# Kernel optimization log

Hardware: AMD Instinct MI355X
Metric: run time of the kernel (lower is better)

The kernel has to match this reference:

```python
import jax, jax.numpy as jnp
import numpy as np

B, D, T, BINS = 8, 768, 16384, 1024

def setup_inputs() -> dict:
    key = jax.random.key(0)
    k1, k2, k3, k4 = jax.random.split(key, 4)
    ssl_content = jax.random.normal(k1, (B, D, T), dtype=jnp.float32)
    conv_w = jax.random.normal(k2, (D, D, 2), dtype=jnp.float32) * 0.02  # Conv1d(768,768,k=2,s=2) weight [out,in,k]
    conv_b = jax.random.normal(k3, (D,), dtype=jnp.float32) * 0.02
    codebook = jax.random.normal(k4, (BINS, D), dtype=jnp.float32)
    return {"ssl_content": ssl_content, "conv_w": conv_w, "conv_b": conv_b, "codebook": codebook}

def reference(ssl_content, conv_w, conv_b, codebook):
    # ssl_proj: Conv1d(D, D, kernel_size=2, stride=2), no padding
    ssl = jax.lax.conv_general_dilated(
        ssl_content, conv_w, window_strides=(2,), padding='VALID',
        dimension_numbers=('NCH', 'OIH', 'NCH')) + conv_b[None, :, None]  # [B, D, T//2]
    x = jnp.transpose(ssl, (0, 2, 1))            # b d n -> b n d : [B, T', D]
    b, tq, d = x.shape
    flat = x.reshape(-1, d)                      # [B*T', D]
    # Euclidean codebook search: argmin_k ||flat - codebook[k]||^2
    d2 = (jnp.sum(flat * flat, axis=-1, keepdims=True)
          - 2.0 * (flat @ codebook.T)
          + jnp.sum(codebook * codebook, axis=-1))  # [B*T', BINS]
    codes = jnp.argmin(d2, axis=-1).reshape(b, tq)  # n_q=1 -> indices for quantizer 0: [B, T']
    prompt = codes[0][None, :]                   # codes[0,0].unsqueeze(0) -> [1, T']
    return prompt
```

## Files before the change

kernel.cpp:

```cpp
#include <hip/hip_runtime.h>

#define D    768
#define T    16384
#define TQ   8192
#define BINS 1024
#define K1   1536
#define NKA  (K1 / 32)
#define NKS  (D / 32)
#define FRAG 1024

typedef _Float16 f16;
typedef _Float16 h8 __attribute__((ext_vector_type(8)));
typedef float    f32x4 __attribute__((ext_vector_type(4)));


__device__ __forceinline__ void gl_lds16(const void* g, void* l) {
    __builtin_amdgcn_global_load_lds(
        (const __attribute__((address_space(1))) void*)g,
        (__attribute__((address_space(3))) void*)l, 16, 0, 0);
}

__global__ __launch_bounds__(64) void cnorm_kernel(const float* __restrict__ cb,
                                                   float* __restrict__ cnorm) {
    int bin  = blockIdx.x;
    int lane = threadIdx.x;
    const float* row = cb + bin * D;
    float s = 0.f;
    for (int k = lane; k < D; k += 64) { float v = row[k]; s += v * v; }
    #pragma unroll
    for (int off = 32; off > 0; off >>= 1) s += __shfl_down(s, off);
    if (lane == 0) cnorm[bin] = s;
}

__global__ __launch_bounds__(256) void pack_b_kernel(
    const float* __restrict__ src, f16* __restrict__ hi, f16* __restrict__ lo,
    int K, int nfrag) {
    int wid = threadIdx.x >> 6, lane = threadIdx.x & 63;
    int fid = blockIdx.x * 4 + wid;
    if (fid >= nfrag) return;
    int nk = K >> 5;
    int r16 = fid / nk, kblk = fid - r16 * nk;
    int row = r16 * 16 + (lane & 15);
    int k0  = kblk * 32 + 8 * (lane >> 4);
    const float* s = src + (size_t)row * K + k0;
    float4 v0 = *(const float4*)s;
    float4 v1 = *(const float4*)(s + 4);
    float vv[8] = {v0.x, v0.y, v0.z, v0.w, v1.x, v1.y, v1.z, v1.w};
    h8 vh, vl;
    #pragma unroll
    for (int j = 0; j < 8; ++j) {
        f16 h = (f16)vv[j];
        vh[j] = h;
        vl[j] = (f16)((vv[j] - (float)h) * 2048.f);
    }
    size_t off = ((size_t)fid * 64 + lane) * 8;
    *(h8*)&hi[off] = vh;
    *(h8*)&lo[off] = vl;
}

__global__ __launch_bounds__(256) void pack_a_kernel(const float* __restrict__ ssl,
                                                     f16* __restrict__ hi,
                                                     f16* __restrict__ lo) {
    int wid = threadIdx.x >> 6, lane = threadIdx.x & 63;
    int kblk = blockIdx.x;
    int l15 = lane & 15, lk = lane >> 4;
    #pragma unroll
    for (int q = 0; q < 2; ++q) {
        int tblk = blockIdx.y * 8 + wid * 2 + q;
        int tp = tblk * 16 + l15;
        int i0 = kblk * 16 + 4 * lk;
        float vv[8];
        #pragma unroll
        for (int ii = 0; ii < 4; ++ii) {
            float2 v = *(const float2*)&ssl[(size_t)(i0 + ii) * T + 2 * tp];
            vv[2 * ii]     = v.x;
            vv[2 * ii + 1] = v.y;
        }
        h8 vh, vl;
        #pragma unroll
        for (int j = 0; j < 8; ++j) {
            f16 h = (f16)vv[j];
            vh[j] = h;
            vl[j] = (f16)((vv[j] - (float)h) * 2048.f);
        }
        size_t off = ((size_t)(tblk * NKA + kblk) * 64 + lane) * 8;
        *(h8*)&hi[off] = vh;
        *(h8*)&lo[off] = vl;
    }
}

__global__ __launch_bounds__(256, 2) void conv_mfma_kernel(
    const f16* __restrict__ Ah, const f16* __restrict__ Al,
    const f16* __restrict__ Bh, const f16* __restrict__ Bl,
    const float* __restrict__ bias,
    f16* __restrict__ Xhi, f16* __restrict__ Xlo)
{
    __shared__ __align__(16) char smem[65536];
    int tid = threadIdx.x, lane = tid & 63, wid = tid >> 6;
    int wm = wid >> 1, wn = wid & 1;
    int l15 = lane & 15, lk = lane >> 4;
    int mb = blockIdx.y * 128, nb = blockIdx.x * 128;
    int mb16 = mb >> 4, nb16 = nb >> 4;

    const f16* gsrc; int blk16;
    if      (wid == 0) { gsrc = Ah; blk16 = mb16; }
    else if (wid == 1) { gsrc = Al; blk16 = mb16; }
    else if (wid == 2) { gsrc = Bh; blk16 = nb16; }
    else               { gsrc = Bl; blk16 = nb16; }
    const char* gw = (const char*)gsrc + (size_t)blk16 * NKA * FRAG + lane * 16;
    char* lw0 = smem + wid * 8192;
    char* lw1 = smem + 32768 + wid * 8192;

    const f32x4 zero4 = {0.f, 0.f, 0.f, 0.f};
    f32x4 acc[4][4], acc2[4][4];
    #pragma unroll
    for (int i = 0; i < 4; ++i)
        #pragma unroll
        for (int j = 0; j < 4; ++j) { acc[i][j] = zero4; acc2[i][j] = zero4; }

    #pragma unroll
    for (int f = 0; f < 8; ++f)
        gl_lds16(gw + (size_t)(f * NKA) * FRAG, lw0 + f * FRAG);
    __syncthreads();

    int cur = 0;
    for (int kblk = 0; kblk < NKA; ++kblk) {
        if (kblk + 1 < NKA) {
            char* lwn = cur ? lw0 : lw1;
            #pragma unroll
            for (int f = 0; f < 8; ++f)
                gl_lds16(gw + (size_t)(f * NKA + kblk + 1) * FRAG, lwn + f * FRAG);
        }
        const char* base = smem + cur * 32768;
        h8 ah[4], al[4];
        #pragma unroll
        for (int mf = 0; mf < 4; ++mf) {
            int fo = (wm * 4 + mf) * FRAG + lane * 16;
            ah[mf] = *(const h8*)(base + fo);
            al[mf] = *(const h8*)(base + 8192 + fo);
        }
        #pragma unroll
        for (int nf = 0; nf < 4; ++nf) {
            int fo = (wn * 4 + nf) * FRAG + lane * 16;
            h8 bh = *(const h8*)(base + 16384 + fo);
            h8 bl = *(const h8*)(base + 24576 + fo);
            #pragma unroll
            for (int mf = 0; mf < 4; ++mf) {
                acc [mf][nf] = __builtin_amdgcn_mfma_f32_16x16x32_f16(ah[mf], bh, acc [mf][nf], 0, 0, 0);
                acc2[mf][nf] = __builtin_amdgcn_mfma_f32_16x16x32_f16(ah[mf], bl, acc2[mf][nf], 0, 0, 0);
                acc2[mf][nf] = __builtin_amdgcn_mfma_f32_16x16x32_f16(al[mf], bh, acc2[mf][nf], 0, 0, 0);
            }
        }
        __syncthreads();
        cur ^= 1;
    }

    float* sb = (float*)smem;
    float bv[4];
    #pragma unroll
    for (int nf = 0; nf < 4; ++nf) bv[nf] = bias[nb + wn * 64 + nf * 16 + l15];
    #pragma unroll
    for (int s = 0; s < 4; ++s) {
        __syncthreads();
        if (wm == (s >> 1)) {
            #pragma unroll
            for (int mh = 0; mh < 2; ++mh) {
                int mf = (s & 1) * 2 + mh;
                int srow = mh * 16 + lk * 4;
                #pragma unroll
                for (int nf = 0; nf < 4; ++nf) {
                    int scol = wn * 64 + nf * 16 + l15;
                    #pragma unroll
                    for (int r = 0; r < 4; ++r)
                        sb[(srow + r) * 132 + scol] =
                            acc[mf][nf][r] + acc2[mf][nf][r] * 4.8828125e-4f + bv[nf];
                }
            }
        }
        __syncthreads();
        #pragma unroll
        for (int h = 0; h < 2; ++h) {
            int f = wid * 2 + h;
            int tl = f & 1, dbl = f >> 1;
            int srow = tl * 16 + l15;
            int sd   = dbl * 32 + 8 * lk;
            float vv[8];
            #pragma unroll
            for (int j = 0; j < 8; ++j) vv[j] = sb[srow * 132 + sd + j];
            h8 vh, vl;
            #pragma unroll
            for (int j = 0; j < 8; ++j) {
                f16 hh = (f16)vv[j];
                vh[j] = hh;
                vl[j] = (f16)((vv[j] - (float)hh) * 2048.f);
            }
            int tblk_g = mb16 + s * 2 + tl;
            int dblk_g = (nb >> 5) + dbl;
            size_t off = ((size_t)(tblk_g * NKS + dblk_g) * 64 + lane) * 8;
            *(h8*)&Xhi[off] = vh;
            *(h8*)&Xlo[off] = vl;
        }
    }
}

__global__ __launch_bounds__(256, 2) void score_mfma_kernel(
    const f16* __restrict__ Ah, const f16* __restrict__ Al,
    const f16* __restrict__ Bh, const f16* __restrict__ Bl,
    const float* __restrict__ cnorm,
    float* __restrict__ pval, int* __restrict__ pidx)
{
    __shared__ __align__(16) char smem[65536];
    int tid = threadIdx.x, lane = tid & 63, wid = tid >> 6;
    int wm = wid >> 1, wn = wid & 1;
    int l15 = lane & 15, lk = lane >> 4;
    int mb = blockIdx.y * 128, nb = blockIdx.x * 128;
    int mb16 = mb >> 4, nb16 = nb >> 4;

    const f16* gsrc; int blk16;
    if      (wid == 0) { gsrc = Ah; blk16 = mb16; }
    else if (wid == 1) { gsrc = Al; blk16 = mb16; }
    else if (wid == 2) { gsrc = Bh; blk16 = nb16; }
    else               { gsrc = Bl; blk16 = nb16; }
    const char* gw = (const char*)gsrc + (size_t)blk16 * NKS * FRAG + lane * 16;
    char* lw0 = smem + wid * 8192;
    char* lw1 = smem + 32768 + wid * 8192;

    const f32x4 zero4 = {0.f, 0.f, 0.f, 0.f};
    f32x4 acc[4][4], acc2[4][4];
    #pragma unroll
    for (int i = 0; i < 4; ++i)
        #pragma unroll
        for (int j = 0; j < 4; ++j) { acc[i][j] = zero4; acc2[i][j] = zero4; }

    #pragma unroll
    for (int f = 0; f < 8; ++f)
        gl_lds16(gw + (size_t)(f * NKS) * FRAG, lw0 + f * FRAG);
    __syncthreads();

    int cur = 0;
    for (int kblk = 0; kblk < NKS; ++kblk) {
        if (kblk + 1 < NKS) {
            char* lwn = cur ? lw0 : lw1;
            #pragma unroll
            for (int f = 0; f < 8; ++f)
                gl_lds16(gw + (size_t)(f * NKS + kblk + 1) * FRAG, lwn + f * FRAG);
        }
        const char* base = smem + cur * 32768;
        h8 ah[4], al[4];
        #pragma unroll
        for (int mf = 0; mf < 4; ++mf) {
            int fo = (wm * 4 + mf) * FRAG + lane * 16;
            ah[mf] = *(const h8*)(base + fo);
            al[mf] = *(const h8*)(base + 8192 + fo);
        }
        #pragma unroll
        for (int nf = 0; nf < 4; ++nf) {
            int fo = (wn * 4 + nf) * FRAG + lane * 16;
            h8 bh = *(const h8*)(base + 16384 + fo);
            h8 bl = *(const h8*)(base + 24576 + fo);
            #pragma unroll
            for (int mf = 0; mf < 4; ++mf) {
                acc [mf][nf] = __builtin_amdgcn_mfma_f32_16x16x32_f16(ah[mf], bh, acc [mf][nf], 0, 0, 0);
                acc2[mf][nf] = __builtin_amdgcn_mfma_f32_16x16x32_f16(ah[mf], bl, acc2[mf][nf], 0, 0, 0);
                acc2[mf][nf] = __builtin_amdgcn_mfma_f32_16x16x32_f16(al[mf], bh, acc2[mf][nf], 0, 0, 0);
            }
        }
        __syncthreads();
        cur ^= 1;
    }
    float cn[4];
    #pragma unroll
    for (int nf = 0; nf < 4; ++nf) cn[nf] = cnorm[nb + wn * 64 + nf * 16 + l15];
    int slice = blockIdx.x * 2 + wn;
    #pragma unroll
    for (int mf = 0; mf < 4; ++mf) {
        #pragma unroll
        for (int r = 0; r < 4; ++r) {
            float v = 3.4e38f; int ix = 0;
            #pragma unroll
            for (int nf = 0; nf < 4; ++nf) {
                float dot = acc[mf][nf][r] + acc2[mf][nf][r] * 4.8828125e-4f;
                float sc = cn[nf] - 2.f * dot;
                int col = nb + wn * 64 + nf * 16 + l15;
                if (sc < v) { v = sc; ix = col; }
            }
            #pragma unroll
            for (int off = 8; off > 0; off >>= 1) {
                float ov = __shfl_xor(v, off);
                int   oi = __shfl_xor(ix, off);
                if (ov < v || (ov == v && oi < ix)) { v = ov; ix = oi; }
            }
            if (l15 == 0) {
                int row = mb + wm * 64 + mf * 16 + lk * 4 + r;
                pval[row * 16 + slice] = v;
                pidx[row * 16 + slice] = ix;
            }
        }
    }
}

__global__ __launch_bounds__(256) void argmin_final_kernel(
    const float* __restrict__ pval, const int* __restrict__ pidx,
    int* __restrict__ out)
{
    int r = blockIdx.x * 256 + threadIdx.x;
    float best = 3.4e38f; int bi = 0;
    #pragma unroll
    for (int s = 0; s < 16; ++s) {
        float v = pval[r * 16 + s];
        if (v < best) { best = v; bi = pidx[r * 16 + s]; }
    }
    out[r] = bi;
}

extern "C" void kernel_launch(void* const* d_in, const int* in_sizes, int n_in,
                              void* d_out, int out_size, void* d_ws, size_t ws_size,
                              hipStream_t stream) {
    const float* ssl = (const float*)d_in[0];
    const float* W   = (const float*)d_in[1];
    const float* bia = (const float*)d_in[2];
    const float* cb  = (const float*)d_in[3];
    int* out = (int*)d_out;

    char* p = (char*)d_ws;
    float* cnorm = (float*)p;  p += 4096;
    f16* Whi  = (f16*)p;  p += (size_t)D * K1 * 2;
    f16* Wlo  = (f16*)p;  p += (size_t)D * K1 * 2;
    f16* CBhi = (f16*)p;  p += (size_t)BINS * D * 2;
    f16* CBlo = (f16*)p;  p += (size_t)BINS * D * 2;
    f16* Ahi  = (f16*)p;  p += (size_t)TQ * K1 * 2;
    f16* Alo  = (f16*)p;  p += (size_t)TQ * K1 * 2;
    f16* Xhi  = (f16*)p;  p += (size_t)TQ * D * 2;
    f16* Xlo  = (f16*)p;  p += (size_t)TQ * D * 2;
    float* pval = (float*)p;  p += (size_t)TQ * 16 * 4;
    int*   pidx = (int*)p;    p += (size_t)TQ * 16 * 4;

    cnorm_kernel<<<BINS, 64, 0, stream>>>(cb, cnorm);
    pack_b_kernel<<<(48 * 48) / 4, 256, 0, stream>>>(W, Whi, Wlo, K1, 48 * 48);
    pack_b_kernel<<<(64 * 24) / 4, 256, 0, stream>>>(cb, CBhi, CBlo, D, 64 * 24);
    pack_a_kernel<<<dim3(NKA, TQ / 128), 256, 0, stream>>>(ssl, Ahi, Alo);
    conv_mfma_kernel<<<dim3(D / 128, TQ / 128), 256, 0, stream>>>(
        Ahi, Alo, Whi, Wlo, bia, Xhi, Xlo);
    score_mfma_kernel<<<dim3(BINS / 128, TQ / 128), 256, 0, stream>>>(
        Xhi, Xlo, CBhi, CBlo, cnorm, pval, pidx);
    argmin_final_kernel<<<TQ / 256, 256, 0, stream>>>(pval, pidx, out);
}
```

Before: 562.0 us.

## Merge prep kernels into one launch and swizzle GEMM block order

Combines the codebook-norm kernel, both B-packing kernels and the A-packing kernel into a single prep kernel that branches on block index, replacing four launches with one. It also remaps the block indices of the conv and score GEMM kernels so that consecutive workgroups are spread across the grid, likely to change L2/MALL locality and how work lands on XCDs. The cost is extra branching in the prep kernel and a different locality pattern that may help or hurt cache reuse.

```diff
diff --git a/kernel.cpp b/kernel.cpp
--- a/kernel.cpp
+++ b/kernel.cpp
@@ -9,6 +9,12 @@
 #define NKS  (D / 32)
 #define FRAG 1024
 
+#define NFRAG_W  ((D / 16) * NKA)
+#define NFRAG_CB ((BINS / 16) * NKS)
+#define NB_PACKB ((NFRAG_W + NFRAG_CB) / 4)
+#define NB_PACKA (NKA * (TQ / 128))
+#define NB_CNORM (BINS / 4)
+
 typedef _Float16 f16;
 typedef _Float16 h8 __attribute__((ext_vector_type(8)));
 typedef float    f32x4 __attribute__((ext_vector_type(4)));
@@ -20,62 +26,29 @@
         (__attribute__((address_space(3))) void*)l, 16, 0, 0);
 }
 
-__global__ __launch_bounds__(64) void cnorm_kernel(const float* __restrict__ cb,
-                                                   float* __restrict__ cnorm) {
-    int bin  = blockIdx.x;
-    int lane = threadIdx.x;
-    const float* row = cb + bin * D;
-    float s = 0.f;
-    for (int k = lane; k < D; k += 64) { float v = row[k]; s += v * v; }
-    #pragma unroll
-    for (int off = 32; off > 0; off >>= 1) s += __shfl_down(s, off);
-    if (lane == 0) cnorm[bin] = s;
-}
-
-__global__ __launch_bounds__(256) void pack_b_kernel(
-    const float* __restrict__ src, f16* __restrict__ hi, f16* __restrict__ lo,
-    int K, int nfrag) {
+__global__ __launch_bounds__(256) void prep_kernel(
+    const float* __restrict__ ssl, const float* __restrict__ W,
+    const float* __restrict__ cb,
+    f16* __restrict__ Whi, f16* __restrict__ Wlo,
+    f16* __restrict__ CBhi, f16* __restrict__ CBlo,
+    f16* __restrict__ Ahi, f16* __restrict__ Alo,
+    float* __restrict__ cnorm)
+{
+    int b = blockIdx.x;
     int wid = threadIdx.x >> 6, lane = threadIdx.x & 63;
-    int fid = blockIdx.x * 4 + wid;
-    if (fid >= nfrag) return;
-    int nk = K >> 5;
-    int r16 = fid / nk, kblk = fid - r16 * nk;
-    int row = r16 * 16 + (lane & 15);
-    int k0  = kblk * 32 + 8 * (lane >> 4);
-    const float* s = src + (size_t)row * K + k0;
-    float4 v0 = *(const float4*)s;
-    float4 v1 = *(const float4*)(s + 4);
-    float vv[8] = {v0.x, v0.y, v0.z, v0.w, v1.x, v1.y, v1.z, v1.w};
-    h8 vh, vl;
-    #pragma unroll
-    for (int j = 0; j < 8; ++j) {
-        f16 h = (f16)vv[j];
-        vh[j] = h;
-        vl[j] = (f16)((vv[j] - (float)h) * 2048.f);
-    }
-    size_t off = ((size_t)fid * 64 + lane) * 8;
-    *(h8*)&hi[off] = vh;
-    *(h8*)&lo[off] = vl;
-}
-
-__global__ __launch_bounds__(256) void pack_a_kernel(const float* __restrict__ ssl,
-                                                     f16* __restrict__ hi,
-                                                     f16* __restrict__ lo) {
-    int wid = threadIdx.x >> 6, lane = threadIdx.x & 63;
-    int kblk = blockIdx.x;
-    int l15 = lane & 15, lk = lane >> 4;
-    #pragma unroll
-    for (int q = 0; q < 2; ++q) {
-        int tblk = blockIdx.y * 8 + wid * 2 + q;
-        int tp = tblk * 16 + l15;
-        int i0 = kblk * 16 + 4 * lk;
-        float vv[8];
-        #pragma unroll
-        for (int ii = 0; ii < 4; ++ii) {
-            float2 v = *(const float2*)&ssl[(size_t)(i0 + ii) * T + 2 * tp];
-            vv[2 * ii]     = v.x;
-            vv[2 * ii + 1] = v.y;
-        }
+
+    if (b < NB_PACKB) {
+        int fid = b * 4 + wid;
+        const float* src; f16* hi; f16* lo; int K, nk, fidl;
+        if (fid < NFRAG_W) { src = W;  hi = Whi;  lo = Wlo;  K = K1; nk = NKA; fidl = fid; }
+        else               { src = cb; hi = CBhi; lo = CBlo; K = D;  nk = NKS; fidl = fid - NFRAG_W; }
+        int r16 = fidl / nk, kblk = fidl - r16 * nk;
+        int row = r16 * 16 + (lane & 15);
+        int k0  = kblk * 32 + 8 * (lane >> 4);
+        const float* s = src + (size_t)row * K + k0;
+        float4 v0 = *(const float4*)s;
+        float4 v1 = *(const float4*)(s + 4);
+        float vv[8] = {v0.x, v0.y, v0.z, v0.w, v1.x, v1.y, v1.z, v1.w};
         h8 vh, vl;
         #pragma unroll
         for (int j = 0; j < 8; ++j) {
@@ -83,9 +56,44 @@
             vh[j] = h;
             vl[j] = (f16)((vv[j] - (float)h) * 2048.f);
         }
-        size_t off = ((size_t)(tblk * NKA + kblk) * 64 + lane) * 8;
+        size_t off = ((size_t)fidl * 64 + lane) * 8;
         *(h8*)&hi[off] = vh;
         *(h8*)&lo[off] = vl;
+    } else if (b < NB_PACKB + NB_PACKA) {
+        int idx = b - NB_PACKB;
+        int kblk = idx % NKA, yb = idx / NKA;
+        int l15 = lane & 15, lk = lane >> 4;
+        #pragma unroll
+        for (int q = 0; q < 2; ++q) {
+            int tblk = yb * 8 + wid * 2 + q;
+            int tp = tblk * 16 + l15;
+            int i0 = kblk * 16 + 4 * lk;
+            float vv[8];
+            #pragma unroll
+            for (int ii = 0; ii < 4; ++ii) {
+                float2 v = *(const float2*)&ssl[(size_t)(i0 + ii) * T + 2 * tp];
+                vv[2 * ii]     = v.x;
+                vv[2 * ii + 1] = v.y;
+            }
+            h8 vh, vl;
+            #pragma unroll
+            for (int j = 0; j < 8; ++j) {
+                f16 h = (f16)vv[j];
+                vh[j] = h;
+                vl[j] = (f16)((vv[j] - (float)h) * 2048.f);
+            }
+            size_t off = ((size_t)(tblk * NKA + kblk) * 64 + lane) * 8;
+            *(h8*)&Ahi[off] = vh;
+            *(h8*)&Alo[off] = vl;
+        }
+    } else {
+        int bin = (b - NB_PACKB - NB_PACKA) * 4 + wid;
+        const float* row = cb + (size_t)bin * D;
+        float s = 0.f;
+        for (int k = lane; k < D; k += 64) { float v = row[k]; s += v * v; }
+        #pragma unroll
+        for (int off = 32; off > 0; off >>= 1) s += __shfl_down(s, off);
+        if (lane == 0) cnorm[bin] = s;
     }
 }
 
@@ -99,7 +107,12 @@
     int tid = threadIdx.x, lane = tid & 63, wid = tid >> 6;
     int wm = wid >> 1, wn = wid & 1;
     int l15 = lane & 15, lk = lane >> 4;
-    int mb = blockIdx.y * 128, nb = blockIdx.x * 128;
+
+    int orig = blockIdx.y * 6 + blockIdx.x;
+    int swz  = (orig & 7) * 48 + (orig >> 3);
+    int bx = swz % 6, by = swz / 6;
+
+    int mb = by * 128, nb = bx * 128;
     int mb16 = mb >> 4, nb16 = nb >> 4;
 
     const f16* gsrc; int blk16;
@@ -213,7 +226,12 @@
     int tid = threadIdx.x, lane = tid & 63, wid = tid >> 6;
     int wm = wid >> 1, wn = wid & 1;
     int l15 = lane & 15, lk = lane >> 4;
-    int mb = blockIdx.y * 128, nb = blockIdx.x * 128;
+
+    int orig = blockIdx.y * 8 + blockIdx.x;
+    int swz  = (orig & 7) * 64 + (orig >> 3);
+    int bx = swz & 7, by = swz >> 3;
+
+    int mb = by * 128, nb = bx * 128;
     int mb16 = mb >> 4, nb16 = nb >> 4;
 
     const f16* gsrc; int blk16;
@@ -271,7 +289,7 @@
     float cn[4];
     #pragma unroll
     for (int nf = 0; nf < 4; ++nf) cn[nf] = cnorm[nb + wn * 64 + nf * 16 + l15];
-    int slice = blockIdx.x * 2 + wn;
+    int slice = bx * 2 + wn;
     #pragma unroll
     for (int mf = 0; mf < 4; ++mf) {
         #pragma unroll
@@ -335,10 +353,8 @@
     float* pval = (float*)p;  p += (size_t)TQ * 16 * 4;
     int*   pidx = (int*)p;    p += (size_t)TQ * 16 * 4;
 
-    cnorm_kernel<<<BINS, 64, 0, stream>>>(cb, cnorm);
-    pack_b_kernel<<<(48 * 48) / 4, 256, 0, stream>>>(W, Whi, Wlo, K1, 48 * 48);
-    pack_b_kernel<<<(64 * 24) / 4, 256, 0, stream>>>(cb, CBhi, CBlo, D, 64 * 24);
-    pack_a_kernel<<<dim3(NKA, TQ / 128), 256, 0, stream>>>(ssl, Ahi, Alo);
+    prep_kernel<<<NB_PACKB + NB_PACKA + NB_CNORM, 256, 0, stream>>>(
+        ssl, W, cb, Whi, Wlo, CBhi, CBlo, Ahi, Alo, cnorm);
     conv_mfma_kernel<<<dim3(D / 128, TQ / 128), 256, 0, stream>>>(
         Ahi, Alo, Whi, Wlo, bia, Xhi, Xlo);
     score_mfma_kernel<<<dim3(BINS / 128, TQ / 128), 256, 0, stream>>>(
```

New measurement: 553.2 us. No clear change (-1.6%).
